# Performance work log

Hardware: AMD Instinct MI355X
Metric: run time of the kernel (lower is better)

Reference implementation:

```python
import jax, jax.numpy as jnp
import numpy as np

B, S, D, H, V, C = 4, 2048, 1024, 16, 32000, 10
FFN_DIM = 2 * D
HD = D // H
SCALE = float(np.sqrt(HD))


def _posenc(seq, d):
    pos = jnp.arange(seq, dtype=jnp.float32)[:, None]
    div = jnp.exp(jnp.arange(0, d, 2, dtype=jnp.float32) * (-np.log(10000.0) / d))
    pe = jnp.zeros((seq, d), dtype=jnp.float32)
    pe = pe.at[:, 0::2].set(jnp.sin(pos * div))
    pe = pe.at[:, 1::2].set(jnp.cos(pos * div))
    return pe


def _layernorm(x, g, b, eps=1e-5):
    mu = jnp.mean(x, axis=-1, keepdims=True)
    var = jnp.mean(jnp.square(x - mu), axis=-1, keepdims=True)
    return (x - mu) * jax.lax.rsqrt(var + eps) * g + b


def setup_inputs() -> dict:
    key = jax.random.key(0)
    ks = jax.random.split(key, 10)
    x_ids = jax.random.randint(ks[0], (B, S), 0, V, dtype=jnp.int64 if jax.config.jax_enable_x64 else jnp.int32)
    mask = jnp.ones((B, S), dtype=jnp.int32)
    emb = (jax.random.normal(ks[1], (V, D), jnp.float32) * 0.02).at[0].set(0.0)  # padding_idx=0
    qkv_w = jax.random.normal(ks[2], (3 * D, D), jnp.float32) * 0.02
    fc_w = jax.random.normal(ks[3], (D, D), jnp.float32) * 0.02
    fc_b = jnp.zeros((D,), jnp.float32)
    ln1_g = jnp.ones((D,), jnp.float32); ln1_b = jnp.zeros((D,), jnp.float32)
    ffn_w1 = jax.random.normal(ks[4], (FFN_DIM, D), jnp.float32) * 0.02
    ffn_b1 = jnp.zeros((FFN_DIM,), jnp.float32)
    ffn_w2 = jax.random.normal(ks[5], (D, FFN_DIM), jnp.float32) * 0.02
    ffn_b2 = jnp.zeros((D,), jnp.float32)
    ln2_g = jnp.ones((D,), jnp.float32); ln2_b = jnp.zeros((D,), jnp.float32)
    pr_w1 = jax.random.normal(ks[6], (D, D), jnp.float32) * 0.02
    pr_b1 = jnp.zeros((D,), jnp.float32)
    pr_w2 = jax.random.normal(ks[7], (C, D), jnp.float32) * 0.02
    pr_b2 = jnp.zeros((C,), jnp.float32)
    return dict(x_ids=x_ids, mask=mask, emb=emb, qkv_w=qkv_w, fc_w=fc_w, fc_b=fc_b,
                ln1_g=ln1_g, ln1_b=ln1_b, ffn_w1=ffn_w1, ffn_b1=ffn_b1,
                ffn_w2=ffn_w2, ffn_b2=ffn_b2, ln2_g=ln2_g, ln2_b=ln2_b,
                pr_w1=pr_w1, pr_b1=pr_b1, pr_w2=pr_w2, pr_b2=pr_b2)


def reference(x_ids, mask, emb, qkv_w, fc_w, fc_b, ln1_g, ln1_b,
              ffn_w1, ffn_b1, ffn_w2, ffn_b2, ln2_g, ln2_b,
              pr_w1, pr_b1, pr_w2, pr_b2):
    # embedding + absolute positional encoding
    x = emb[x_ids] + _posenc(S, D)  # [B,S,D]
    residual = x
    # multi-head attention (dropout is identity at eval)
    qkv = jnp.einsum('bsd,ed->bse', x, qkv_w)  # [B,S,3D]
    q, k, v = jnp.split(qkv, 3, axis=-1)
    q = q.reshape(B, S, H, HD)
    k = k.reshape(B, S, H, HD)
    v = v.reshape(B, S, H, HD)
    attn = jnp.einsum('bqhd,bkhd->bhqk', q, k) / SCALE  # [B,H,S,S]
    attn = jnp.where(mask[:, None, None, :] == 0, -jnp.inf, attn)
    attn = jax.nn.softmax(attn, axis=-1)
    o = jnp.einsum('bhqk,bkhd->bqhd', attn, v).reshape(B, S, D)
    o = jnp.einsum('bsd,ed->bse', o, fc_w) + fc_b
    x = _layernorm(o + residual, ln1_g, ln1_b)
    # FFN block (residual + LayerNorm inside)
    h = jax.nn.gelu(jnp.einsum('bsd,fd->bsf', x, ffn_w1) + ffn_b1, approximate=False)
    h = jnp.einsum('bsf,df->bsd', h, ffn_w2) + ffn_b2
    x = _layernorm(h + x, ln2_g, ln2_b)
    # masked max-pool over sequence
    x = jnp.where(mask[:, :, None] == 0, -jnp.inf, x).max(axis=1)  # [B,D]
    # prediction head
    h = jax.nn.gelu(x @ pr_w1.T + pr_b1, approximate=False)
    logits = h @ pr_w2.T + pr_b2  # [B,C]
    return logits
```

## Files before the change

kernel.cpp:

```cpp
#include <hip/hip_runtime.h>
#include <math.h>

#define B_   4
#define S_   2048
#define D_   1024
#define H_   16
#define HD_  64
#define C_   10
#define FFN_ 2048
#define M_   (B_ * S_)
#define D3_  (3 * D_)

typedef unsigned short u16;
typedef __bf16 bf16x8 __attribute__((ext_vector_type(8)));
typedef float  f32x4  __attribute__((ext_vector_type(4)));

#define EXPSCL 0.18033688011112042f

__device__ __forceinline__ u16 f2bf(float f) {
  union { float f; unsigned u; } x; x.f = f;
  unsigned r = x.u + 0x7fffu + ((x.u >> 16) & 1u);
  return (u16)(r >> 16);
}
__device__ __forceinline__ unsigned cvtpk(float lo, float hi) {
  unsigned r;
  asm("v_cvt_pk_bf16_f32 %0, %1, %2" : "=v"(r) : "v"(lo), "v"(hi));
  return r;
}
__device__ __forceinline__ float gelu_f(float x) {
  return 0.5f * x * (1.f + erff(x * 0.70710678118654752440f));
}
__device__ __forceinline__ void gload_lds16(const void* g, void* l) {
  __builtin_amdgcn_global_load_lds(
      (const __attribute__((address_space(1))) unsigned int*)g,
      (__attribute__((address_space(3))) unsigned int*)l, 16, 0, 0);
}
__device__ __forceinline__ bf16x8 ldsfrag(const u16* buf, int rowbase, int fr, int kb) {
  return *(const bf16x8*)&buf[(rowbase + fr) * 64 + ((kb ^ (fr & 7)) << 3)];
}

#define CV0 786432
#define CV1 262144
#define CV2 524288
#define CV3 524288
__global__ __launch_bounds__(256) void prep_kernel(const float* __restrict__ s0,
                                                   const float* __restrict__ s1,
                                                   const float* __restrict__ s2,
                                                   const float* __restrict__ s3,
                                                   u16* __restrict__ d0,
                                                   u16* __restrict__ d1,
                                                   u16* __restrict__ d2,
                                                   u16* __restrict__ d3,
                                                   const int* __restrict__ ids,
                                                   const float* __restrict__ emb,
                                                   float* __restrict__ resid,
                                                   u16* __restrict__ xb) {
  if (blockIdx.x < 8192) {
    int v = blockIdx.x * 256 + threadIdx.x;
    const float* s; u16* d;
    if (v < CV0) { s = s0; d = d0; }
    else if (v < CV0 + CV1) { s = s1; d = d1; v -= CV0; }
    else if (v < CV0 + CV1 + CV2) { s = s2; d = d2; v -= CV0 + CV1; }
    else { s = s3; d = d3; v -= CV0 + CV1 + CV2; }
    const int i = v * 4;
    f32x4 x = *(const f32x4*)&s[i];
    ushort4 o;
    o.x = f2bf(x[0]); o.y = f2bf(x[1]); o.z = f2bf(x[2]); o.w = f2bf(x[3]);
    *(ushort4*)&d[i] = o;
  } else {
    const int m  = blockIdx.x - 8192;
    const int s  = m & (S_ - 1);
    const int id = ids[m];
    const int d4 = threadIdx.x * 4;
    const f32x4 e = *(const f32x4*)&emb[(size_t)id * D_ + d4];
    const float fs = (float)s;
    const float f0 = __expf((float)d4 * (-9.210340371976184f / 1024.0f));
    const float f1 = __expf((float)(d4 + 2) * (-9.210340371976184f / 1024.0f));
    float s0v, c0v, s1v, c1v;
    __sincosf(fs * f0, &s0v, &c0v);
    __sincosf(fs * f1, &s1v, &c1v);
    f32x4 v;
    v[0] = e[0] + s0v; v[1] = e[1] + c0v; v[2] = e[2] + s1v; v[3] = e[3] + c1v;
    *(f32x4*)&resid[(size_t)m * D_ + d4] = v;
    ushort4 pk;
    pk.x = f2bf(v[0]); pk.y = f2bf(v[1]); pk.z = f2bf(v[2]); pk.w = f2bf(v[3]);
    *(ushort4*)&xb[(size_t)m * D_ + d4] = pk;
  }
}

template <int BIAS, int GELU, int OUTBF, int QSCALE, int VSPLIT>
__global__ __launch_bounds__(256) void gemm_bt(const u16* __restrict__ A,
                                               const u16* __restrict__ W,
                                               const float* __restrict__ bias,
                                               float* __restrict__ outf,
                                               u16* __restrict__ outb,
                                               u16* __restrict__ vtout,
                                               int M, int N, int K) {
  __shared__ u16 As[128 * 64];
  __shared__ u16 Bs[128 * 64];
  const int tid  = threadIdx.x;
  const int lane = tid & 63;
  const int w    = tid >> 6;
  const int nx  = gridDim.x;
  const int nwg = nx * gridDim.y;
  int t = blockIdx.y * nx + blockIdx.x;
  t = (t & 7) * (nwg >> 3) + (t >> 3);
  const int bx = t % nx, by = t / nx;
  const int l3   = lane >> 3;
  const int sb   = (lane & 7) ^ l3;
  const u16* Ag0 = A + (size_t)(by * 128 + w * 32 + l3) * K + sb * 8;
  const u16* Wg0 = W + (size_t)(bx * 128 + w * 32 + l3) * K + sb * 8;

  f32x4 acc[4][4] = {};
  const int wr  = (w & 1) * 64;
  const int wc  = (w >> 1) * 64;
  const int fr  = lane & 15;
  const int fq  = lane >> 4;

  for (int kt = 0; kt < K; kt += 64) {
#pragma unroll
    for (int c = 0; c < 4; ++c) {
      gload_lds16(Ag0 + (size_t)(c * 8) * K + kt, &As[(w * 32 + c * 8) * 64]);
      gload_lds16(Wg0 + (size_t)(c * 8) * K + kt, &Bs[(w * 32 + c * 8) * 64]);
    }
    __syncthreads();
#pragma unroll
    for (int ks = 0; ks < 2; ++ks) {
      const int kb = ks * 4 + fq;
      bf16x8 af[4], bfr[4];
#pragma unroll
      for (int i = 0; i < 4; ++i) af[i] = ldsfrag(As, wr + i * 16, fr, kb);
#pragma unroll
      for (int j = 0; j < 4; ++j) bfr[j] = ldsfrag(Bs, wc + j * 16, fr, kb);
#pragma unroll
      for (int i = 0; i < 4; ++i)
#pragma unroll
        for (int j = 0; j < 4; ++j)
          acc[i][j] = __builtin_amdgcn_mfma_f32_16x16x32_bf16(bfr[j], af[i], acc[i][j], 0, 0, 0);
    }
    __syncthreads();
  }

  const float qs = (QSCALE && bx < 8) ? EXPSCL : 1.f;
#pragma unroll
  for (int i = 0; i < 4; ++i) {
    const int m = by * 128 + wr + i * 16 + fr;
#pragma unroll
    for (int j = 0; j < 4; ++j) {
      const int nb = bx * 128 + wc + j * 16 + fq * 4;
      f32x4 v = acc[i][j];
      if (BIAS) v += *(const f32x4*)&bias[nb];
      if (GELU) {
        v[0] = gelu_f(v[0]); v[1] = gelu_f(v[1]);
        v[2] = gelu_f(v[2]); v[3] = gelu_f(v[3]);
      }
      if (QSCALE) v *= qs;
      if (VSPLIT && bx >= 16) {
        const int hh = (nb - 2 * D_) >> 6;
        const int dl = (nb - 2 * D_) & 63;
        const int bb = m >> 11, ss = m & (S_ - 1);
        u16* vdst = vtout + ((size_t)((bb * H_ + hh) * 64 + dl)) * S_ + ss;
        vdst[0]          = f2bf(v[0]);
        vdst[(size_t)S_]     = f2bf(v[1]);
        vdst[(size_t)2 * S_] = f2bf(v[2]);
        vdst[(size_t)3 * S_] = f2bf(v[3]);
      } else if (OUTBF) {
        ushort4 pk;
        pk.x = f2bf(v[0]); pk.y = f2bf(v[1]); pk.z = f2bf(v[2]); pk.w = f2bf(v[3]);
        *(ushort4*)&outb[(size_t)m * N + nb] = pk;
      } else {
        *(f32x4*)&outf[(size_t)m * N + nb] = v;
      }
    }
  }
}

__global__ __launch_bounds__(512) void attn_mfma_kernel(const u16* __restrict__ qkv,
                                                        const u16* __restrict__ vt,
                                                        const int* __restrict__ mask,
                                                        u16* __restrict__ attno) {
  __shared__ u16 Ks[64 * 64];
  __shared__ u16 Vts[64 * 64];
  __shared__ u16 Ps[8][16 * 64];
  const int tid = threadIdx.x, lane = tid & 63, w = tid >> 6;
  int t = (blockIdx.z * 16 + blockIdx.y) * 16 + blockIdx.x;
  t = (t & 7) * 128 + (t >> 3);
  const int qt = t & 15, h = (t >> 4) & 15, b = t >> 8;
  const int l3 = lane >> 3;
  const int sb = (lane & 7) ^ l3;
  const int fr = lane & 15, fq = lane >> 4;
  u16* PsFlat = &Ps[0][0];

  {
    const u16* qbase = qkv + (size_t)(b * S_ + qt * 128 + w * 16) * D3_ + h * 64 + sb * 8;
    gload_lds16(qbase + (size_t)l3 * D3_, &PsFlat[(w * 16) * 64]);
    gload_lds16(qbase + (size_t)(8 + l3) * D3_, &PsFlat[(w * 16 + 8) * 64]);
  }

  bool ALLV;
  {
    const int4* mp = (const int4*)&mask[b * S_];
    int mv = 1;
#pragma unroll
    for (int tt = 0; tt < 8; ++tt) {
      const int4 m4 = mp[tt * 64 + lane];
      mv &= (m4.x != 0) & (m4.y != 0) & (m4.z != 0) & (m4.w != 0);
    }
    ALLV = (__ballot(mv != 0) == ~0ull);
  }

  __syncthreads();

  bf16x8 qf[2];
#pragma unroll
  for (int ks = 0; ks < 2; ++ks)
    qf[ks] = ldsfrag(PsFlat, w * 16, fr, ks * 4 + fq);

  __syncthreads();

  float l_st = 0.f;
  f32x4 ot[4] = {};
  u16* PsW = Ps[w];

  for (int kt = 0; kt < S_ / 64; ++kt) {
    {
      const u16* kbase = qkv + (size_t)(b * S_ + kt * 64 + w * 8 + l3) * D3_ + D_ + h * 64 + sb * 8;
      gload_lds16(kbase, &Ks[(w * 8) * 64]);
      const u16* vbase = vt + ((size_t)((b * H_ + h) * 64 + w * 8 + l3)) * S_ + kt * 64 + sb * 8;
      gload_lds16(vbase, &Vts[(w * 8) * 64]);
    }
    __syncthreads();

    f32x4 sf[4] = {};
#pragma unroll
    for (int ks = 0; ks < 2; ++ks) {
      const int kb = ks * 4 + fq;
      __builtin_amdgcn_s_setprio(1);
#pragma unroll
      for (int r4 = 0; r4 < 4; ++r4) {
        bf16x8 kf = ldsfrag(Ks, r4 * 16, fr, kb);
        sf[r4] = __builtin_amdgcn_mfma_f32_16x16x32_bf16(kf, qf[ks], sf[r4], 0, 0, 0);
      }
      __builtin_amdgcn_s_setprio(0);
    }
    if (!ALLV) {
#pragma unroll
      for (int r4 = 0; r4 < 4; ++r4) {
        const int4 mm = *(const int4*)&mask[b * S_ + kt * 64 + r4 * 16 + fq * 4];
        f32x4 vb;
        vb[0] = mm.x ? 0.f : -1e30f;
        vb[1] = mm.y ? 0.f : -1e30f;
        vb[2] = mm.z ? 0.f : -1e30f;
        vb[3] = mm.w ? 0.f : -1e30f;
        sf[r4] += vb;
      }
    }

    {
      u16* pw = PsW + fr * 64;
      float sum = l_st;
#pragma unroll
      for (int r4 = 0; r4 < 4; ++r4) {
        const float p0 = __builtin_exp2f(sf[r4][0]);
        const float p1 = __builtin_exp2f(sf[r4][1]);
        const float p2 = __builtin_exp2f(sf[r4][2]);
        const float p3 = __builtin_exp2f(sf[r4][3]);
        sum += (p0 + p1) + (p2 + p3);
        const int bk0 = 2 * r4 + (fq >> 1);
        const int off = ((bk0 ^ (fr & 7)) << 3) + ((fq & 1) << 2);
        uint2 pk; pk.x = cvtpk(p0, p1); pk.y = cvtpk(p2, p3);
        *(uint2*)&pw[off] = pk;
      }
      l_st = sum;
    }
    asm volatile("s_waitcnt lgkmcnt(0)" ::: "memory");

#pragma unroll
    for (int ks = 0; ks < 2; ++ks) {
      const int kb = ks * 4 + fq;
      bf16x8 pf = ldsfrag(PsW, 0, fr, kb);
      __builtin_amdgcn_s_setprio(1);
#pragma unroll
      for (int db = 0; db < 4; ++db) {
        bf16x8 vf = ldsfrag(Vts, db * 16, fr, kb);
        ot[db] = __builtin_amdgcn_mfma_f32_16x16x32_bf16(vf, pf, ot[db], 0, 0, 0);
      }
      __builtin_amdgcn_s_setprio(0);
    }
    __syncthreads();
  }

  {
    float l = l_st;
    l += __shfl_xor(l, 16);
    l += __shfl_xor(l, 32);
    const float inv = (l > 0.f) ? 1.f / l : 0.f;
    const int qrow = qt * 128 + w * 16 + fr;
    u16* dst = attno + (size_t)(b * S_ + qrow) * D_ + h * 64 + fq * 4;
#pragma unroll
    for (int db = 0; db < 4; ++db) {
      ushort4 pk;
      pk.x = f2bf(ot[db][0] * inv);
      pk.y = f2bf(ot[db][1] * inv);
      pk.z = f2bf(ot[db][2] * inv);
      pk.w = f2bf(ot[db][3] * inv);
      *(ushort4*)&dst[db * 16] = pk;
    }
  }
}

template <int WRITEB>
__global__ __launch_bounds__(256) void ln_kernel(const float* __restrict__ a,
                                                 const float* __restrict__ res,
                                                 const float* __restrict__ g,
                                                 const float* __restrict__ be,
                                                 float* __restrict__ outf,
                                                 u16* __restrict__ outb) {
  const int row = blockIdx.x, tid = threadIdx.x;
  const int lane = tid & 63, w = tid >> 6;
  const size_t base = (size_t)row * D_ + tid * 4;
  const f32x4 va = *(const f32x4*)(a + base);
  const f32x4 vr = *(const f32x4*)(res + base);
  const f32x4 v  = va + vr;
  float s = v[0] + v[1] + v[2] + v[3];
#pragma unroll
  for (int o = 32; o > 0; o >>= 1) s += __shfl_xor(s, o);
  __shared__ float red[8];
  if (lane == 0) red[w] = s;
  __syncthreads();
  const float mu = (red[0] + red[1] + red[2] + red[3]) * (1.f / D_);
  const f32x4 d = v - mu;
  float s2 = d[0] * d[0] + d[1] * d[1] + d[2] * d[2] + d[3] * d[3];
#pragma unroll
  for (int o = 32; o > 0; o >>= 1) s2 += __shfl_xor(s2, o);
  if (lane == 0) red[4 + w] = s2;
  __syncthreads();
  const float var = (red[4] + red[5] + red[6] + red[7]) * (1.f / D_);
  const float rs = rsqrtf(var + 1e-5f);
  f32x4 y;
#pragma unroll
  for (int k = 0; k < 4; ++k) {
    const int ch = tid * 4 + k;
    y[k] = d[k] * rs * g[ch] + be[ch];
  }
  *(f32x4*)&outf[base] = y;
  if (WRITEB) {
    ushort4 pk;
    pk.x = f2bf(y[0]); pk.y = f2bf(y[1]); pk.z = f2bf(y[2]); pk.w = f2bf(y[3]);
    *(ushort4*)&outb[base] = pk;
  }
}

__global__ __launch_bounds__(256) void pool_part_kernel(const float* __restrict__ x,
                                                        const int* __restrict__ mask,
                                                        float* __restrict__ part) {
  const int b = blockIdx.y, ch = blockIdx.x;
  const int d0 = threadIdx.x * 4;
  f32x4 acc = {-INFINITY, -INFINITY, -INFINITY, -INFINITY};
  for (int ss = 0; ss < 64; ++ss) {
    const int s = ch * 64 + ss;
    if (mask[b * S_ + s] != 0) {
      const f32x4 v = *(const f32x4*)&x[(size_t)(b * S_ + s) * D_ + d0];
      acc[0] = fmaxf(acc[0], v[0]);
      acc[1] = fmaxf(acc[1], v[1]);
      acc[2] = fmaxf(acc[2], v[2]);
      acc[3] = fmaxf(acc[3], v[3]);
    }
  }
  *(f32x4*)&part[(size_t)(b * 32 + ch) * D_ + d0] = acc;
}
__global__ __launch_bounds__(256) void pool_final_kernel(const float* __restrict__ part,
                                                         float* __restrict__ pooled) {
  const int b = blockIdx.x;
  const int d0 = threadIdx.x * 4;
  f32x4 acc = {-INFINITY, -INFINITY, -INFINITY, -INFINITY};
  for (int ch = 0; ch < 32; ++ch) {
    const f32x4 v = *(const f32x4*)&part[(size_t)(b * 32 + ch) * D_ + d0];
    acc[0] = fmaxf(acc[0], v[0]);
    acc[1] = fmaxf(acc[1], v[1]);
    acc[2] = fmaxf(acc[2], v[2]);
    acc[3] = fmaxf(acc[3], v[3]);
  }
  *(f32x4*)&pooled[(size_t)b * D_ + d0] = acc;
}

__global__ __launch_bounds__(256) void head1_kernel(const float* __restrict__ pooled,
                                                    const float* __restrict__ w,
                                                    const float* __restrict__ bias,
                                                    float* __restrict__ hh) {
  const int lane = threadIdx.x & 63;
  const int gw = blockIdx.x * 4 + (threadIdx.x >> 6);
  const int b = gw >> 10, n = gw & 1023;
  const float* p  = pooled + b * 1024;
  const float* wr = w + (size_t)n * 1024;
  float s = 0.f;
  for (int d = lane; d < 1024; d += 64) s += p[d] * wr[d];
#pragma unroll
  for (int off = 32; off > 0; off >>= 1) s += __shfl_xor(s, off);
  if (lane == 0) hh[b * 1024 + n] = gelu_f(s + bias[n]);
}
__global__ __launch_bounds__(256) void head2_kernel(const float* __restrict__ hh,
                                                    const float* __restrict__ w,
                                                    const float* __restrict__ bias,
                                                    float* __restrict__ out) {
  const int lane = threadIdx.x & 63;
  const int gw = blockIdx.x * 4 + (threadIdx.x >> 6);
  const int b = gw / 10, c = gw % 10;
  const float* p  = hh + b * 1024;
  const float* wr = w + (size_t)c * 1024;
  float s = 0.f;
  for (int d = lane; d < 1024; d += 64) s += p[d] * wr[d];
#pragma unroll
  for (int off = 32; off > 0; off >>= 1) s += __shfl_xor(s, off);
  if (lane == 0) out[b * 10 + c] = s + bias[c];
}

#define OFF_RESID  0UL
#define OFF_F1     33554432UL
#define OFF_XB     67108864UL
#define OFF_QKVB   83886080UL
#define OFF_ATTNO  134217728UL
#define OFF_WQKV   150994944UL
#define OFF_WFC    157286400UL
#define OFF_WF1    159383552UL
#define OFF_WF2    163577856UL
#define OFF_PART   167772160UL
#define OFF_POOLED 168296448UL
#define OFF_HH     168312832UL

extern "C" void kernel_launch(void* const* d_in, const int* in_sizes, int n_in,
                              void* d_out, int out_size, void* d_ws, size_t ws_size,
                              hipStream_t stream) {
  const int*   x_ids  = (const int*)d_in[0];
  const int*   mask   = (const int*)d_in[1];
  const float* emb    = (const float*)d_in[2];
  const float* qkv_w  = (const float*)d_in[3];
  const float* fc_w   = (const float*)d_in[4];
  const float* fc_b   = (const float*)d_in[5];
  const float* ln1_g  = (const float*)d_in[6];
  const float* ln1_b  = (const float*)d_in[7];
  const float* ffn_w1 = (const float*)d_in[8];
  const float* ffn_b1 = (const float*)d_in[9];
  const float* ffn_w2 = (const float*)d_in[10];
  const float* ffn_b2 = (const float*)d_in[11];
  const float* ln2_g  = (const float*)d_in[12];
  const float* ln2_b  = (const float*)d_in[13];
  const float* pr_w1  = (const float*)d_in[14];
  const float* pr_b1  = (const float*)d_in[15];
  const float* pr_w2  = (const float*)d_in[16];
  const float* pr_b2  = (const float*)d_in[17];
  float* out = (float*)d_out;
  char* ws = (char*)d_ws;

  float* resid  = (float*)(ws + OFF_RESID);
  float* f1     = (float*)(ws + OFF_F1);
  u16*   vtb    = (u16*)(ws + OFF_F1);
  u16*   xb     = (u16*)(ws + OFF_XB);
  u16*   qkvb   = (u16*)(ws + OFF_QKVB);
  u16*   hb     = (u16*)(ws + OFF_QKVB);
  u16*   attnob = (u16*)(ws + OFF_ATTNO);
  u16*   wqkvb  = (u16*)(ws + OFF_WQKV);
  u16*   wfcb   = (u16*)(ws + OFF_WFC);
  u16*   wf1b   = (u16*)(ws + OFF_WF1);
  u16*   wf2b   = (u16*)(ws + OFF_WF2);
  float* part   = (float*)(ws + OFF_PART);
  float* pooled = (float*)(ws + OFF_POOLED);
  float* hh     = (float*)(ws + OFF_HH);

  prep_kernel<<<16384, 256, 0, stream>>>(qkv_w, fc_w, ffn_w1, ffn_w2,
                                         wqkvb, wfcb, wf1b, wf2b,
                                         x_ids, emb, resid, xb);

  gemm_bt<0, 0, 1, 1, 1><<<dim3(D3_ / 128, M_ / 128), 256, 0, stream>>>(
      xb, wqkvb, nullptr, nullptr, qkvb, vtb, M_, D3_, D_);

  attn_mfma_kernel<<<dim3(S_ / 128, H_, B_), 512, 0, stream>>>(qkvb, vtb, mask, attnob);

  gemm_bt<1, 0, 0, 0, 0><<<dim3(D_ / 128, M_ / 128), 256, 0, stream>>>(
      attnob, wfcb, fc_b, f1, nullptr, nullptr, M_, D_, D_);

  ln_kernel<1><<<M_, 256, 0, stream>>>(f1, resid, ln1_g, ln1_b, resid, xb);

  gemm_bt<1, 1, 1, 0, 0><<<dim3(FFN_ / 128, M_ / 128), 256, 0, stream>>>(
      xb, wf1b, ffn_b1, nullptr, hb, nullptr, M_, FFN_, D_);

  gemm_bt<1, 0, 0, 0, 0><<<dim3(D_ / 128, M_ / 128), 256, 0, stream>>>(
      hb, wf2b, ffn_b2, f1, nullptr, nullptr, M_, D_, FFN_);

  ln_kernel<0><<<M_, 256, 0, stream>>>(f1, resid, ln2_g, ln2_b, f1, nullptr);

  pool_part_kernel<<<dim3(32, B_), 256, 0, stream>>>(f1, mask, part);
  pool_final_kernel<<<B_, 256, 0, stream>>>(part, pooled);

  head1_kernel<<<1024, 256, 0, stream>>>(pooled, pr_w1, pr_b1, hh);
  head2_kernel<<<10, 256, 0, stream>>>(hh, pr_w2, pr_b2, out);
}
```

Measured before the change: 599.1 us.

## Add 256x256-tile 8-wave pipelined GEMM for QKV and FFN1 projections

```diff
diff --git a/kernel.cpp b/kernel.cpp
--- a/kernel.cpp
+++ b/kernel.cpp
@@ -88,6 +88,133 @@
   }
 }
 
+template <int BIAS, int GELU, int QSCALE, int VSPLIT>
+__global__ __launch_bounds__(512) void gemm256(const u16* __restrict__ A,
+                                               const u16* __restrict__ W,
+                                               const float* __restrict__ bias,
+                                               u16* __restrict__ outb,
+                                               u16* __restrict__ vtout,
+                                               int M, int N, int K) {
+  __shared__ u16 lds[2][4][128 * 64];
+  const int tid = threadIdx.x, lane = tid & 63, w = tid >> 6;
+  const int nx = gridDim.x, nwg = nx * gridDim.y;
+  int t = blockIdx.y * nx + blockIdx.x;
+  t = (t & 7) * (nwg >> 3) + (t >> 3);
+  const int bx = t % nx, by = t / nx;
+  const int l3 = lane >> 3, sb = (lane & 7) ^ l3;
+  const int fr = lane & 15, fq = lane >> 4;
+  const int wm = w >> 2, wn = w & 3;
+  const u16* Ag = A + (size_t)(by * 256 + w * 16 + l3) * K + sb * 8;
+  const u16* Wg = W + (size_t)(bx * 256 + w * 16 + l3) * K + sb * 8;
+  const int NT = K >> 6;
+
+#define ST_A(tt, bb, h)                                                       \
+  do {                                                                        \
+    const u16* g_ = Ag + (size_t)((h) * 128) * K + (size_t)(tt) * 64;         \
+    gload_lds16(g_, &lds[bb][h][(w * 16) * 64]);                              \
+    gload_lds16(g_ + (size_t)8 * K, &lds[bb][h][(w * 16 + 8) * 64]);          \
+  } while (0)
+#define ST_B(tt, bb, h)                                                       \
+  do {                                                                        \
+    const u16* g_ = Wg + (size_t)((h) * 128) * K + (size_t)(tt) * 64;         \
+    gload_lds16(g_, &lds[bb][2 + (h)][(w * 16) * 64]);                        \
+    gload_lds16(g_ + (size_t)8 * K, &lds[bb][2 + (h)][(w * 16 + 8) * 64]);    \
+  } while (0)
+
+  ST_A(0, 0, 0); ST_A(0, 0, 1); ST_B(0, 0, 0); ST_B(0, 0, 1);
+  ST_B(1, 1, 0); ST_B(1, 1, 1);
+  asm volatile("s_waitcnt vmcnt(4)" ::: "memory");
+  __builtin_amdgcn_s_barrier();
+
+  f32x4 acc[8][4] = {};
+  bf16x8 bf[4][2];
+  const int cb = (wn & 1) * 64;
+
+#define PHASE(p, ...)                                                         \
+  {                                                                           \
+    if ((p) == 0) {                                                           \
+      _Pragma("unroll") for (int n = 0; n < 4; ++n) {                         \
+        _Pragma("unroll") for (int kk = 0; kk < 2; ++kk) {                    \
+          bf[n][kk] = ldsfrag(Bs_, cb + n * 16, fr, kk * 4 + fq);             \
+        }                                                                     \
+      }                                                                       \
+    }                                                                         \
+    bf16x8 af[2][2];                                                          \
+    _Pragma("unroll") for (int mm = 0; mm < 2; ++mm) {                        \
+      _Pragma("unroll") for (int kk = 0; kk < 2; ++kk) {                      \
+        af[mm][kk] = ldsfrag(As_, (2 * (p) + mm) * 16, fr, kk * 4 + fq);      \
+      }                                                                       \
+    }                                                                         \
+    __VA_ARGS__;                                                              \
+    __builtin_amdgcn_s_barrier();                                             \
+    asm volatile("s_waitcnt lgkmcnt(0)" ::: "memory");                        \
+    __builtin_amdgcn_sched_barrier(0);                                        \
+    __builtin_amdgcn_s_setprio(1);                                            \
+    _Pragma("unroll") for (int mm = 0; mm < 2; ++mm) {                        \
+      _Pragma("unroll") for (int n = 0; n < 4; ++n) {                         \
+        _Pragma("unroll") for (int kk = 0; kk < 2; ++kk) {                    \
+          acc[2 * (p) + mm][n] = __builtin_amdgcn_mfma_f32_16x16x32_bf16(     \
+              bf[n][kk], af[mm][kk], acc[2 * (p) + mm][n], 0, 0, 0);          \
+        }                                                                     \
+      }                                                                       \
+    }                                                                         \
+    __builtin_amdgcn_s_setprio(0);                                            \
+  }
+
+  for (int g = 0; g < NT; ++g) {
+    const int b = g & 1;
+    const u16* As_ = lds[b][wm];
+    const u16* Bs_ = lds[b][2 + (wn >> 1)];
+
+    PHASE(0, if (g + 1 < NT) ST_A(g + 1, b ^ 1, 0));
+    __builtin_amdgcn_s_barrier();
+    PHASE(1, if (g + 1 < NT) ST_A(g + 1, b ^ 1, 1));
+    __builtin_amdgcn_s_barrier();
+    PHASE(2, if (g + 2 < NT) ST_B(g + 2, b, 0));
+    __builtin_amdgcn_s_barrier();
+    PHASE(3, if (g + 2 < NT) ST_B(g + 2, b, 1));
+    if (g + 1 < NT) {
+      if (g + 2 < NT) { asm volatile("s_waitcnt vmcnt(4)" ::: "memory"); }
+      else            { asm volatile("s_waitcnt vmcnt(0)" ::: "memory"); }
+    }
+    __builtin_amdgcn_s_barrier();
+  }
+#undef PHASE
+#undef ST_A
+#undef ST_B
+
+  const float qs = (QSCALE && bx < 4) ? EXPSCL : 1.f;
+#pragma unroll
+  for (int m = 0; m < 8; ++m) {
+    const int mrow = by * 256 + wm * 128 + m * 16 + fr;
+#pragma unroll
+    for (int n = 0; n < 4; ++n) {
+      const int ncol = bx * 256 + wn * 64 + n * 16 + fq * 4;
+      f32x4 v = acc[m][n];
+      if (BIAS) v += *(const f32x4*)&bias[ncol];
+      if (GELU) {
+        v[0] = gelu_f(v[0]); v[1] = gelu_f(v[1]);
+        v[2] = gelu_f(v[2]); v[3] = gelu_f(v[3]);
+      }
+      if (QSCALE) v *= qs;
+      if (VSPLIT && bx >= 8) {
+        const int hh = (ncol - 2 * D_) >> 6;
+        const int dl = (ncol - 2 * D_) & 63;
+        const int bb2 = mrow >> 11, ss = mrow & (S_ - 1);
+        u16* vdst = vtout + ((size_t)((bb2 * H_ + hh) * 64 + dl)) * S_ + ss;
+        vdst[0]              = f2bf(v[0]);
+        vdst[(size_t)S_]     = f2bf(v[1]);
+        vdst[(size_t)2 * S_] = f2bf(v[2]);
+        vdst[(size_t)3 * S_] = f2bf(v[3]);
+      } else {
+        ushort4 pk;
+        pk.x = f2bf(v[0]); pk.y = f2bf(v[1]); pk.z = f2bf(v[2]); pk.w = f2bf(v[3]);
+        *(ushort4*)&outb[(size_t)mrow * N + ncol] = pk;
+      }
+    }
+  }
+}
+
 template <int BIAS, int GELU, int OUTBF, int QSCALE, int VSPLIT>
 __global__ __launch_bounds__(256) void gemm_bt(const u16* __restrict__ A,
                                                const u16* __restrict__ W,
@@ -471,8 +598,8 @@
                                          wqkvb, wfcb, wf1b, wf2b,
                                          x_ids, emb, resid, xb);
 
-  gemm_bt<0, 0, 1, 1, 1><<<dim3(D3_ / 128, M_ / 128), 256, 0, stream>>>(
-      xb, wqkvb, nullptr, nullptr, qkvb, vtb, M_, D3_, D_);
+  gemm256<0, 0, 1, 1><<<dim3(D3_ / 256, M_ / 256), 512, 0, stream>>>(
+      xb, wqkvb, nullptr, qkvb, vtb, M_, D3_, D_);
 
   attn_mfma_kernel<<<dim3(S_ / 128, H_, B_), 512, 0, stream>>>(qkvb, vtb, mask, attnob);
 
@@ -481,8 +608,8 @@
 
   ln_kernel<1><<<M_, 256, 0, stream>>>(f1, resid, ln1_g, ln1_b, resid, xb);
 
-  gemm_bt<1, 1, 1, 0, 0><<<dim3(FFN_ / 128, M_ / 128), 256, 0, stream>>>(
-      xb, wf1b, ffn_b1, nullptr, hb, nullptr, M_, FFN_, D_);
+  gemm256<1, 1, 0, 0><<<dim3(FFN_ / 256, M_ / 256), 512, 0, stream>>>(
+      xb, wf1b, ffn_b1, hb, nullptr, M_, FFN_, D_);
 
   gemm_bt<1, 0, 0, 0, 0><<<dim3(D_ / 128, M_ / 128), 256, 0, stream>>>(
       hb, wf2b, ffn_b2, f1, nullptr, nullptr, M_, D_, FFN_);
```

Measured after the change: 608.0 us. Within noise of the previous version (+1.5%).
